# Kernel optimization log

Hardware: AMD Instinct MI355X
Metric: run time of the kernel (lower is better)

Reference implementation:

```python
import jax, jax.numpy as jnp
import numpy as np

N = 100000      # number of agents/nodes
T = 512         # number of timesteps (edges has T-1 steps)
E = 1024        # edge_per_t
MU = 0.05       # diffusion rate (init kwarg mu)
RHO = 32.0      # sigmoid sharpness (init kwarg rho)


def setup_inputs() -> dict:
    key = jax.random.key(0)
    k1, k2, k3, k4, k5 = jax.random.split(key, 5)
    logit_X0 = jax.random.normal(k1, (N,), dtype=jnp.float32)
    theta = jax.random.normal(k2, (1,), dtype=jnp.float32)
    u = jax.random.randint(k3, (T - 1, E), 0, N)
    v = jax.random.randint(k4, (T - 1, E), 0, N)
    s = jax.random.randint(k5, (T - 1, E), 0, 2)  # activation flag in {0,1}
    edges = jnp.stack([u, v, s], axis=-1).astype(jnp.int32)  # [T-1, E, 3]
    return {"logit_X0": logit_X0, "theta": theta, "edges": edges}


def reference(logit_X0, theta, edges):
    X0 = jax.nn.sigmoid(logit_X0)          # [N]
    epsilon = jax.nn.sigmoid(theta)         # [1]

    def step(X_t, e):
        # e: [E, 3] -> (u, v, s). Gather-diff-scale-scatter update.
        u, v = e[:, 0], e[:, 1]
        s = e[:, 2].astype(X_t.dtype)
        d = (X_t[u] - X_t[v]) * s           # [E]
        upd = jnp.zeros_like(X_t).at[u].add(-d).at[v].add(d)
        X_next = X_t + MU * upd
        return X_next, X_next

    _, Xs = jax.lax.scan(step, X0, edges)   # Xs: [T-1, N]
    X = jnp.concatenate([X0[None, :], Xs], axis=0)  # [T, N]

    # diff_X = X[t, u] - X[t, v] with t = step index (state before update)
    Xp = X[:-1]                              # [T-1, N]
    diff = (jnp.take_along_axis(Xp, edges[:, :, 0], axis=1)
            - jnp.take_along_axis(Xp, edges[:, :, 1], axis=1))  # [T-1, E]
    kappa = jax.nn.sigmoid(RHO * (epsilon - jnp.abs(diff.reshape(-1))))
    return X, kappa
```

## Files before the change

### kernel.cpp

```cpp
#include <hip/hip_runtime.h>
#include <math.h>

#define NN 100000
#define TT 512
#define EE 1024
#define NSTEP (TT - 1)
#define NE (NSTEP * EE)
#define NCHUNK (NE / 256)
#define FLOWG 512
#define MU 0.05f
#define RHO 32.0f
#define CAP (NE * 2)
#define NOTREADY 0xFFFFFFFFu
#define SCAN_BLK 1024
#define SCAN_NB ((NN + SCAN_BLK - 1) / SCAN_BLK)
#define RB 32
#define NRC (TT / RB)
#define FILL_BX ((NN / 4 + 255) / 256)

#define AGT __HIP_MEMORY_SCOPE_AGENT
#define WGS __HIP_MEMORY_SCOPE_WORKGROUP
#define RLX __ATOMIC_RELAXED

__device__ __forceinline__ float sigmoid_f(float x) {
    return 1.0f / (1.0f + expf(-x));
}

__device__ __forceinline__ unsigned try_val(const unsigned* pub, int p) {
    return __hip_atomic_load((unsigned*)&pub[p], RLX, AGT);
}
__device__ __forceinline__ void publish(unsigned* pub, int p, float v) {
    __hip_atomic_store(&pub[p], __float_as_uint(v), RLX, AGT);
}

__device__ __forceinline__ int lower_bound(const unsigned* __restrict__ a,
                                           int lo, int hi, unsigned key) {
    while (lo < hi) {
        int mid = (lo + hi) >> 1;
        if (a[mid] < key) lo = mid + 1; else hi = mid;
    }
    return lo;
}

__global__ void k_init(const float* __restrict__ logit, float* __restrict__ X0f,
                       float* __restrict__ out, int* __restrict__ cnt,
                       int* __restrict__ cur) {
    int n = blockIdx.x * blockDim.x + threadIdx.x;
    if (n < NN) {
        float x = sigmoid_f(logit[n]);
        X0f[n] = x;
        out[n] = x;
        cnt[n] = 0;
        cur[n] = 0;
    }
}

__global__ void k_count(const int* __restrict__ edges, int* __restrict__ cnt,
                        unsigned* __restrict__ pub) {
    int i = blockIdx.x * blockDim.x + threadIdx.x;
    if (i < NE) {
        pub[2 * i]     = NOTREADY;
        pub[2 * i + 1] = NOTREADY;
        int s = edges[3 * i + 2];
        if (s) {
            atomicAdd(&cnt[edges[3 * i + 0]], 1);
            atomicAdd(&cnt[edges[3 * i + 1]], 1);
        }
    }
}

__global__ void __launch_bounds__(256) k_scanA(const int* __restrict__ cnt,
                                               int* __restrict__ bsum) {
    __shared__ int sh[256];
    const int t = threadIdx.x;
    const int base = blockIdx.x * SCAN_BLK + t * 4;
    int s = 0;
    if (base + 3 < NN) {
        const int4 v = *(const int4*)(cnt + base);
        s = v.x + v.y + v.z + v.w;
    } else {
        for (int k = 0; k < 4; ++k) if (base + k < NN) s += cnt[base + k];
    }
    sh[t] = s;
    __syncthreads();
    for (int o = 128; o > 0; o >>= 1) {
        if (t < o) sh[t] += sh[t + o];
        __syncthreads();
    }
    if (t == 0) bsum[blockIdx.x] = sh[0];
}

__global__ void __launch_bounds__(128) k_scanB(int* __restrict__ bsum) {
    __shared__ int sh[128];
    const int t = threadIdx.x;
    int v = (t < SCAN_NB) ? bsum[t] : 0;
    sh[t] = v;
    __syncthreads();
    for (int o = 1; o < 128; o <<= 1) {
        int x = (t >= o) ? sh[t - o] : 0;
        __syncthreads();
        sh[t] += x;
        __syncthreads();
    }
    if (t < SCAN_NB) bsum[t] = sh[t] - v;
}

__global__ void __launch_bounds__(256) k_scanC(const int* __restrict__ cnt,
                                               const int* __restrict__ bsum,
                                               int* __restrict__ off) {
    __shared__ int sh[256];
    const int t = threadIdx.x;
    const int base = blockIdx.x * SCAN_BLK + t * 4;
    int a0 = 0, a1 = 0, a2 = 0, a3 = 0;
    if (base + 3 < NN) {
        const int4 v = *(const int4*)(cnt + base);
        a0 = v.x; a1 = v.y; a2 = v.z; a3 = v.w;
    } else {
        if (base + 0 < NN) a0 = cnt[base + 0];
        if (base + 1 < NN) a1 = cnt[base + 1];
        if (base + 2 < NN) a2 = cnt[base + 2];
    }
    const int s = a0 + a1 + a2 + a3;
    sh[t] = s;
    __syncthreads();
    for (int o = 1; o < 256; o <<= 1) {
        int x = (t >= o) ? sh[t - o] : 0;
        __syncthreads();
        sh[t] += x;
        __syncthreads();
    }
    int ex = sh[t] - s + bsum[blockIdx.x];
    if (base + 3 < NN) {
        int4 w; w.x = ex; w.y = ex + a0; w.z = ex + a0 + a1; w.w = ex + a0 + a1 + a2;
        *(int4*)(off + base) = w;
    } else {
        if (base + 0 < NN) off[base + 0] = ex;
        if (base + 1 < NN) off[base + 1] = ex + a0;
        if (base + 2 < NN) off[base + 2] = ex + a0 + a1;
    }
}

__global__ void k_place(const int* __restrict__ edges,
                        const int* __restrict__ off, int* __restrict__ cur,
                        unsigned* __restrict__ ent) {
    int i = blockIdx.x * blockDim.x + threadIdx.x;
    if (i < NE) {
        int s = edges[3 * i + 2];
        if (s) {
            int u = edges[3 * i + 0];
            int v = edges[3 * i + 1];
            unsigned key = ((unsigned)i) << 1;
            ent[off[u] + atomicAdd(&cur[u], 1)] = key;
            ent[off[v] + atomicAdd(&cur[v], 1)] = key | 1u;
        }
    }
}

__global__ void k_sort(const int* __restrict__ off, const int* __restrict__ cur,
                       unsigned* __restrict__ ent) {
    int n = blockIdx.x * blockDim.x + threadIdx.x;
    if (n >= NN) return;
    int lo = off[n], c = cur[n];
    for (int k = 1; k < c; ++k) {
        unsigned key = ent[lo + k];
        int j = k;
        while (j > 0 && ent[lo + j - 1] > key) {
            ent[lo + j] = ent[lo + j - 1];
            --j;
        }
        ent[lo + j] = key;
    }
}

__global__ void __launch_bounds__(256, 2)
k_flow(const int* __restrict__ edges, const float* __restrict__ theta,
       const float* __restrict__ X0f, const int* __restrict__ off,
       const int* __restrict__ cur, const unsigned* __restrict__ ent,
       unsigned* __restrict__ pub, float* __restrict__ out_kappa) {
    const float eps = sigmoid_f(theta[0]);
    for (int c = blockIdx.x; c < NCHUNK; c += gridDim.x) {
        const int i = (c << 8) + threadIdx.x;
        const int t = i >> 10;
        const int u = edges[3 * i + 0];
        const int v = edges[3 * i + 1];
        const int s = edges[3 * i + 2];

        const unsigned stepkey = ((unsigned)t) << 11;

        const int lu = off[u], hu = lu + cur[u];
        const int qu = lower_bound(ent, lu, hu, stepkey);
        const int lv = off[v], hv = lv + cur[v];
        const int qv = lower_bound(ent, lv, hv, stepkey);

        int mu_ = -1, mv_ = -1;
        if (s) {
            const unsigned ku = ((unsigned)i) << 1;
            mu_ = qu; while (ent[mu_] != ku) ++mu_;
            const unsigned kv = ku | 1u;
            mv_ = qv; while (ent[mv_] != kv) ++mv_;
        }

        bool have_xu = (qu == lu);
        bool have_xv = (qv == lv);
        float xu = have_xu ? X0f[u] : 0.0f;
        float xv = have_xv ? X0f[v] : 0.0f;
        bool m_rdy = false;
        bool pu_done = (s == 0);
        bool pv_done = (s == 0);
        float m = 0.0f, diff = 0.0f;
        int tries = 0;

        while (!(m_rdy && pu_done && pv_done)) {
            if (!have_xu) {
                unsigned w = try_val(pub, qu - 1);
                if (w != NOTREADY) { xu = __uint_as_float(w); have_xu = true; }
            }
            if (!have_xv) {
                unsigned w = try_val(pub, qv - 1);
                if (w != NOTREADY) { xv = __uint_as_float(w); have_xv = true; }
            }
            if (have_xu && have_xv && !m_rdy) {
                diff = xu - xv;
                m = MU * diff;
                m_rdy = true;
            }
            if (m_rdy && !pu_done) {
                if (mu_ == qu) { publish(pub, mu_, xu - m); pu_done = true; }
                else {
                    unsigned w = try_val(pub, mu_ - 1);
                    if (w != NOTREADY) {
                        publish(pub, mu_, __uint_as_float(w) - m);
                        pu_done = true;
                    }
                }
            }
            if (m_rdy && !pv_done) {
                if (mv_ == qv) { publish(pub, mv_, xv + m); pv_done = true; }
                else {
                    unsigned w = try_val(pub, mv_ - 1);
                    if (w != NOTREADY) {
                        publish(pub, mv_, __uint_as_float(w) + m);
                        pv_done = true;
                    }
                }
            }
            if (!(m_rdy && pu_done && pv_done)) {
                ++tries;
                if (tries > 24)     __builtin_amdgcn_s_sleep(4);
                else if (tries > 6) __builtin_amdgcn_s_sleep(2);
            }
        }
        out_kappa[i] = sigmoid_f(RHO * (eps - fabsf(diff)));
    }
}

__global__ void __launch_bounds__(256) k_fill_pub(float* __restrict__ out,
                                                  const float* __restrict__ X0f,
                                                  const int* __restrict__ off,
                                                  const int* __restrict__ cur,
                                                  const unsigned* __restrict__ ent,
                                                  const unsigned* __restrict__ pub) {
    const int n0 = (blockIdx.x * 256 + threadIdx.x) * 4;
    if (n0 >= NN) return;
    const int r0 = blockIdx.y * RB;
    const unsigned key0 = ((unsigned)r0) << 11;

    int   p[4], e2[4];
    unsigned nxt[4];
    float val[4];
    #pragma unroll
    for (int j = 0; j < 4; ++j) {
        const int n = n0 + j;
        const int lo = off[n];
        e2[j] = lo + cur[n];
        int q = lower_bound(ent, lo, e2[j], key0);
        val[j] = (q > lo) ? __uint_as_float(pub[q - 1]) : X0f[n];
        p[j] = q;
        nxt[j] = (q < e2[j]) ? ent[q] : 0xFFFFFFFFu;
    }

    const int rstart = (r0 == 0) ? 1 : r0;
    for (int r = rstart; r < r0 + RB; ++r) {
        const unsigned lim = ((unsigned)r) << 11;
        #pragma unroll
        for (int j = 0; j < 4; ++j) {
            while (nxt[j] < lim) {
                val[j] = __uint_as_float(pub[p[j]]);
                ++p[j];
                nxt[j] = (p[j] < e2[j]) ? ent[p[j]] : 0xFFFFFFFFu;
            }
        }
        float4 w; w.x = val[0]; w.y = val[1]; w.z = val[2]; w.w = val[3];
        *(float4*)(out + (size_t)r * NN + n0) = w;
    }
}

__global__ void __launch_bounds__(1024) k_seq(const int* __restrict__ edges,
                                              const float* __restrict__ theta,
                                              float* __restrict__ X,
                                              float* __restrict__ out_kappa,
                                              float* __restrict__ md) {
    const int tid = threadIdx.x;
    const float eps = sigmoid_f(theta[0]);
    int u = edges[3 * tid + 0];
    int v = edges[3 * tid + 1];
    int s = edges[3 * tid + 2];
    for (int t = 0; t < NSTEP; ++t) {
        int nu = 0, nv = 0, ns = 0;
        if (t + 1 < NSTEP) {
            const int nb = (t + 1) * 3 * EE + 3 * tid;
            nu = edges[nb + 0]; nv = edges[nb + 1]; ns = edges[nb + 2];
        }
        float xu = __hip_atomic_load(&X[u], RLX, WGS);
        float xv = __hip_atomic_load(&X[v], RLX, WGS);
        float diff = xu - xv;
        out_kappa[t * EE + tid] = sigmoid_f(RHO * (eps - fabsf(diff)));
        bool act = (s && diff != 0.0f);
        float m = act ? MU * diff : 0.0f;
        md[t * EE + tid] = m;
        __syncthreads();
        if (act) {
            __hip_atomic_fetch_add(&X[u], -m, RLX, WGS);
            __hip_atomic_fetch_add(&X[v],  m, RLX, WGS);
        }
        __syncthreads();
        u = nu; v = nv; s = ns;
    }
}

__global__ void k_fill_md(float* __restrict__ out,
                          const int* __restrict__ off, const int* __restrict__ cur,
                          const unsigned* __restrict__ ent,
                          const float* __restrict__ md) {
    int n = blockIdx.x * blockDim.x + threadIdx.x;
    if (n >= NN) return;
    float val = out[n];
    int p = off[n];
    const int e2 = p + cur[n];
    unsigned nxt = (p < e2) ? ent[p] : 0xFFFFFFFFu;
    for (int r = 1; r < TT; ++r) {
        const unsigned lim = ((unsigned)r) << 11;
        while (nxt < lim) {
            float m = md[nxt >> 1];
            val += (nxt & 1u) ? m : -m;
            ++p;
            nxt = (p < e2) ? ent[p] : 0xFFFFFFFFu;
        }
        out[(size_t)r * NN + n] = val;
    }
}

extern "C" void kernel_launch(void* const* d_in, const int* in_sizes, int n_in,
                              void* d_out, int out_size, void* d_ws, size_t ws_size,
                              hipStream_t stream) {
    const float* logit = (const float*)d_in[0];
    const float* theta = (const float*)d_in[1];
    const int*   edges = (const int*)d_in[2];
    float* out = (float*)d_out;
    float* kap = out + (size_t)TT * NN;

    char* ws = (char*)d_ws;
    float*    X0f  = (float*)ws;    ws += sizeof(float) * NN;
    int*      cnt  = (int*)ws;      ws += sizeof(int) * NN;
    int*      off  = (int*)ws;      ws += sizeof(int) * NN;
    int*      cur  = (int*)ws;      ws += sizeof(int) * NN;
    int*      bsum = (int*)ws;      ws += sizeof(int) * ((SCAN_NB + 3) & ~3);
    unsigned* ent  = (unsigned*)ws; ws += sizeof(unsigned) * CAP;
    unsigned* pub = (unsigned*)ws;
    float*    md  = (float*)ws;

    const size_t need_main = (size_t)(4 * NN + SCAN_NB + 3) * 4
                           + (size_t)CAP * 4 * 2;
    const bool main_path = ws_size >= need_main;

    k_init <<<(NN + 255) / 256, 256, 0, stream>>>(logit, X0f, out, cnt, cur);
    k_count<<<(NE + 255) / 256, 256, 0, stream>>>(edges, cnt, pub);
    k_scanA<<<SCAN_NB, 256, 0, stream>>>(cnt, bsum);
    k_scanB<<<1, 128, 0, stream>>>(bsum);
    k_scanC<<<SCAN_NB, 256, 0, stream>>>(cnt, bsum, off);
    k_place<<<(NE + 255) / 256, 256, 0, stream>>>(edges, off, cur, ent);
    k_sort <<<(NN + 255) / 256, 256, 0, stream>>>(off, cur, ent);

    bool flow_ok = false;
    if (main_path) {
        const int* a_edges = edges; const float* a_theta = theta;
        const float* a_x0 = X0f; const int* a_off = off; const int* a_cur = cur;
        const unsigned* a_ent = ent; unsigned* a_pub = pub; float* a_kap = kap;
        void* args[] = { &a_edges, &a_theta, &a_x0, &a_off, &a_cur,
                         &a_ent, &a_pub, &a_kap };
        hipError_t e = hipLaunchCooperativeKernel((const void*)k_flow,
                                                  dim3(FLOWG), dim3(256),
                                                  args, 0, stream);
        if (e == hipSuccess) {
            flow_ok = true;
            k_fill_pub<<<dim3(FILL_BX, NRC), 256, 0, stream>>>(out, X0f, off,
                                                               cur, ent, pub);
        } else {
            (void)hipGetLastError();
        }
    }
    if (!flow_ok) {
        k_seq<<<1, 1024, 0, stream>>>(edges, theta, X0f, kap, md);
        k_fill_md<<<(NN + 255) / 256, 256, 0, stream>>>(out, off, cur, ent, md);
    }
}
```

Baseline: 248.9 us.

## Launch one flow block per chunk, merge small prep kernels, use nontemporal stores

Raises the cooperative flow kernel grid to one block per 256-edge chunk (NCHUNK blocks) with launch bounds allowing 8 blocks per CU, and falls back to the previous 512-block grid if the cooperative launch fails. Folds the pub initialization into k_init and the block-sum scan into k_scanC, which removes one kernel launch. Switches the output fill in k_fill_pub to nontemporal stores. The larger grid relies on the launch succeeding with enough co-resident blocks, and the tighter launch bounds may force register spills. The redundant per-block scan of the block sums in k_scanC adds a little work to every block.

```diff
diff --git a/kernel.cpp b/kernel.cpp
--- a/kernel.cpp
+++ b/kernel.cpp
@@ -7,7 +7,8 @@
 #define NSTEP (TT - 1)
 #define NE (NSTEP * EE)
 #define NCHUNK (NE / 256)
-#define FLOWG 512
+#define FLOWG_FULL NCHUNK
+#define FLOWG_HALF 512
 #define MU 0.05f
 #define RHO 32.0f
 #define CAP (NE * 2)
@@ -22,6 +23,8 @@
 #define WGS __HIP_MEMORY_SCOPE_WORKGROUP
 #define RLX __ATOMIC_RELAXED
 
+typedef float f32x4 __attribute__((ext_vector_type(4)));
+
 __device__ __forceinline__ float sigmoid_f(float x) {
     return 1.0f / (1.0f + expf(-x));
 }
@@ -44,23 +47,24 @@
 
 __global__ void k_init(const float* __restrict__ logit, float* __restrict__ X0f,
                        float* __restrict__ out, int* __restrict__ cnt,
-                       int* __restrict__ cur) {
-    int n = blockIdx.x * blockDim.x + threadIdx.x;
-    if (n < NN) {
-        float x = sigmoid_f(logit[n]);
-        X0f[n] = x;
-        out[n] = x;
-        cnt[n] = 0;
-        cur[n] = 0;
-    }
-}
-
-__global__ void k_count(const int* __restrict__ edges, int* __restrict__ cnt,
-                        unsigned* __restrict__ pub) {
+                       int* __restrict__ cur, unsigned* __restrict__ pub) {
     int i = blockIdx.x * blockDim.x + threadIdx.x;
     if (i < NE) {
         pub[2 * i]     = NOTREADY;
         pub[2 * i + 1] = NOTREADY;
+        if (i < NN) {
+            float x = sigmoid_f(logit[i]);
+            X0f[i] = x;
+            out[i] = x;
+            cnt[i] = 0;
+            cur[i] = 0;
+        }
+    }
+}
+
+__global__ void k_count(const int* __restrict__ edges, int* __restrict__ cnt) {
+    int i = blockIdx.x * blockDim.x + threadIdx.x;
+    if (i < NE) {
         int s = edges[3 * i + 2];
         if (s) {
             atomicAdd(&cnt[edges[3 * i + 0]], 1);
@@ -90,26 +94,23 @@
     if (t == 0) bsum[blockIdx.x] = sh[0];
 }
 
-__global__ void __launch_bounds__(128) k_scanB(int* __restrict__ bsum) {
-    __shared__ int sh[128];
-    const int t = threadIdx.x;
-    int v = (t < SCAN_NB) ? bsum[t] : 0;
-    sh[t] = v;
-    __syncthreads();
-    for (int o = 1; o < 128; o <<= 1) {
-        int x = (t >= o) ? sh[t - o] : 0;
-        __syncthreads();
-        sh[t] += x;
-        __syncthreads();
-    }
-    if (t < SCAN_NB) bsum[t] = sh[t] - v;
-}
-
 __global__ void __launch_bounds__(256) k_scanC(const int* __restrict__ cnt,
                                                const int* __restrict__ bsum,
                                                int* __restrict__ off) {
     __shared__ int sh[256];
+    __shared__ int sb[128];
     const int t = threadIdx.x;
+
+    if (t < 128) sb[t] = (t < SCAN_NB) ? bsum[t] : 0;
+    __syncthreads();
+    for (int o = 1; o < 128; o <<= 1) {
+        int x = (t < 128 && t >= o) ? sb[t - o] : 0;
+        __syncthreads();
+        if (t < 128) sb[t] += x;
+        __syncthreads();
+    }
+    const int boff = (blockIdx.x == 0) ? 0 : sb[blockIdx.x - 1];
+
     const int base = blockIdx.x * SCAN_BLK + t * 4;
     int a0 = 0, a1 = 0, a2 = 0, a3 = 0;
     if (base + 3 < NN) {
@@ -129,7 +130,7 @@
         sh[t] += x;
         __syncthreads();
     }
-    int ex = sh[t] - s + bsum[blockIdx.x];
+    int ex = sh[t] - s + boff;
     if (base + 3 < NN) {
         int4 w; w.x = ex; w.y = ex + a0; w.z = ex + a0 + a1; w.w = ex + a0 + a1 + a2;
         *(int4*)(off + base) = w;
@@ -172,7 +173,7 @@
     }
 }
 
-__global__ void __launch_bounds__(256, 2)
+__global__ void __launch_bounds__(256, 8)
 k_flow(const int* __restrict__ edges, const float* __restrict__ theta,
        const float* __restrict__ X0f, const int* __restrict__ off,
        const int* __restrict__ cur, const unsigned* __restrict__ ent,
@@ -290,8 +291,8 @@
                 nxt[j] = (p[j] < e2[j]) ? ent[p[j]] : 0xFFFFFFFFu;
             }
         }
-        float4 w; w.x = val[0]; w.y = val[1]; w.z = val[2]; w.w = val[3];
-        *(float4*)(out + (size_t)r * NN + n0) = w;
+        f32x4 w; w.x = val[0]; w.y = val[1]; w.z = val[2]; w.w = val[3];
+        __builtin_nontemporal_store(w, (f32x4*)(out + (size_t)r * NN + n0));
     }
 }
 
@@ -373,10 +374,9 @@
                            + (size_t)CAP * 4 * 2;
     const bool main_path = ws_size >= need_main;
 
-    k_init <<<(NN + 255) / 256, 256, 0, stream>>>(logit, X0f, out, cnt, cur);
-    k_count<<<(NE + 255) / 256, 256, 0, stream>>>(edges, cnt, pub);
+    k_init <<<(NE + 255) / 256, 256, 0, stream>>>(logit, X0f, out, cnt, cur, pub);
+    k_count<<<(NE + 255) / 256, 256, 0, stream>>>(edges, cnt);
     k_scanA<<<SCAN_NB, 256, 0, stream>>>(cnt, bsum);
-    k_scanB<<<1, 128, 0, stream>>>(bsum);
     k_scanC<<<SCAN_NB, 256, 0, stream>>>(cnt, bsum, off);
     k_place<<<(NE + 255) / 256, 256, 0, stream>>>(edges, off, cur, ent);
     k_sort <<<(NN + 255) / 256, 256, 0, stream>>>(off, cur, ent);
@@ -389,8 +389,14 @@
         void* args[] = { &a_edges, &a_theta, &a_x0, &a_off, &a_cur,
                          &a_ent, &a_pub, &a_kap };
         hipError_t e = hipLaunchCooperativeKernel((const void*)k_flow,
-                                                  dim3(FLOWG), dim3(256),
+                                                  dim3(FLOWG_FULL), dim3(256),
                                                   args, 0, stream);
+        if (e != hipSuccess) {
+            (void)hipGetLastError();
+            e = hipLaunchCooperativeKernel((const void*)k_flow,
+                                           dim3(FLOWG_HALF), dim3(256),
+                                           args, 0, stream);
+        }
         if (e == hipSuccess) {
             flow_ok = true;
             k_fill_pub<<<dim3(FILL_BX, NRC), 256, 0, stream>>>(out, X0f, off,
```

New measurement: 305.4 us. 1.23x slower.
